# Optimization experiments

Hardware: AMD Instinct MI355X
Metric: run time of the kernel (lower is better)

The kernel has to match this reference:

```python
import jax, jax.numpy as jnp
import numpy as np

NUM_TOKENS = 16384
DIM = 4096
N_EXPERTS = 256
ROUTE_SCALE = 1.0


def setup_inputs() -> dict:
    key = jax.random.key(0)
    k_x, k_w = jax.random.split(key)
    x = jax.random.normal(k_x, (NUM_TOKENS, DIM), dtype=jnp.float32)
    # nn.init.normal_(weight, std=0.02)
    weight = 0.02 * jax.random.normal(k_w, (N_EXPERTS, DIM), dtype=jnp.float32)
    return {"x": x, "weight": weight}


def reference(x, weight):
    # Router GEMM: [T, D] @ [D, E] -> [T, E]
    scores = jnp.einsum("td,ed->te", x, weight)
    # Eval-mode token_choice path: softmax in fp32
    probs = jax.nn.softmax(scores.astype(jnp.float32), axis=-1)  # [T, E]
    indices = jnp.argmax(probs, axis=-1, keepdims=True)  # [T, 1] int
    # Hard one-hot scatter of argmax
    y_hard = jax.nn.one_hot(indices[:, 0], N_EXPERTS, dtype=probs.dtype)  # [T, E]
    # Straight-through estimator mix
    ste = jax.lax.stop_gradient(y_hard - probs) + probs
    # Gather routing weight at the selected expert
    weights = jnp.take_along_axis(ste, indices, axis=-1)  # [T, 1]
    weights = (weights * ROUTE_SCALE).astype(x.dtype)
    return weights, indices
```

## Files before the change

### kernel.cpp

```cpp
#include <hip/hip_runtime.h>
#include <stdint.h>

#define NUM_TOKENS 16384
#define DIM        4096
#define NEXP       256
#define MB         64
#define BK         64
#define APAD       72
#define NWAVES     8
#define MARGIN     0.025f
#define CAP        16384

typedef __attribute__((ext_vector_type(4))) float   f32x4;
typedef __attribute__((ext_vector_type(8))) __bf16  bf16x8;
typedef __attribute__((ext_vector_type(8))) unsigned short u16x8;

static __device__ __forceinline__ unsigned short f32_to_bf16(float f) {
    unsigned int u = __float_as_uint(f);
    u += 0x7fffu + ((u >> 16) & 1u);
    return (unsigned short)(u >> 16);
}

__global__ void cvt_weights(const float* __restrict__ w,
                            unsigned short* __restrict__ wh,
                            int* __restrict__ counter) {
    if (blockIdx.x == 0 && threadIdx.x == 0) *counter = 0;
    const int n4 = NEXP * DIM / 4;
    const int stride = gridDim.x * blockDim.x;
    for (int i = blockIdx.x * blockDim.x + threadIdx.x; i < n4; i += stride) {
        float4 v = ((const float4*)w)[i];
        ushort4 h;
        h.x = f32_to_bf16(v.x); h.y = f32_to_bf16(v.y);
        h.z = f32_to_bf16(v.z); h.w = f32_to_bf16(v.w);
        ((ushort4*)wh)[i] = h;
    }
}

__global__ __launch_bounds__(512, 2) void gate_main(
    const float* __restrict__ x,
    const unsigned short* __restrict__ wh,
    float* __restrict__ out,
    int* __restrict__ counter,
    int4* __restrict__ entries)
{
    __shared__ unsigned short lAh[2][MB][APAD];
    __shared__ unsigned short lBh[2][NEXP * BK];
    __shared__ float4 cand[NWAVES][MB];

    const int tid  = threadIdx.x;
    const int wv   = tid >> 6;
    const int lane = tid & 63;
    const int tok0 = blockIdx.x * MB;

    const int ta   = tid >> 3;
    const int kseg = (tid & 7) * 8;
    const float* xrow = x + (size_t)(tok0 + ta) * DIM + kseg;

    const int esub   = lane >> 3;
    const int bk_off = ((lane & 7) ^ esub) * 8;

    const int quad = lane >> 4;
    const int col  = lane & 15;

    f32x4 acc[4][2];
    #pragma unroll
    for (int mt = 0; mt < 4; ++mt) {
        acc[mt][0] = f32x4{0.f, 0.f, 0.f, 0.f};
        acc[mt][1] = f32x4{0.f, 0.f, 0.f, 0.f};
    }

    {
        #pragma unroll
        for (int jj = 0; jj < 4; ++jj) {
            const int e = jj * 64 + wv * 8 + esub;
            const unsigned short* gh = wh + (size_t)e * DIM + bk_off;
            unsigned short* dh = &lBh[0][jj * 4096 + wv * 512];
            __builtin_amdgcn_global_load_lds(
                (const __attribute__((address_space(1))) unsigned int*)gh,
                (__attribute__((address_space(3))) unsigned int*)dh, 16, 0, 0);
        }
        float4 v0 = *(const float4*)(xrow);
        float4 v1 = *(const float4*)(xrow + 4);
        u16x8 vh;
        vh[0] = f32_to_bf16(v0.x); vh[1] = f32_to_bf16(v0.y);
        vh[2] = f32_to_bf16(v0.z); vh[3] = f32_to_bf16(v0.w);
        vh[4] = f32_to_bf16(v1.x); vh[5] = f32_to_bf16(v1.y);
        vh[6] = f32_to_bf16(v1.z); vh[7] = f32_to_bf16(v1.w);
        *(u16x8*)&lAh[0][ta][kseg] = vh;
        __syncthreads();
    }

    int cur = 0;
    for (int k0 = 0; k0 < DIM; k0 += BK) {
        const int nxt = cur ^ 1;
        const bool has_next = (k0 + BK) < DIM;
        float4 v0, v1;

        if (has_next) {
            #pragma unroll
            for (int jj = 0; jj < 4; ++jj) {
                const int e = jj * 64 + wv * 8 + esub;
                const unsigned short* gh = wh + (size_t)e * DIM + (k0 + BK) + bk_off;
                unsigned short* dh = &lBh[nxt][jj * 4096 + wv * 512];
                __builtin_amdgcn_global_load_lds(
                    (const __attribute__((address_space(1))) unsigned int*)gh,
                    (__attribute__((address_space(3))) unsigned int*)dh, 16, 0, 0);
            }
            v0 = *(const float4*)(xrow + k0 + BK);
            v1 = *(const float4*)(xrow + k0 + BK + 4);
        }

        #pragma unroll
        for (int kk = 0; kk < BK; kk += 32) {
            const int kc = kk >> 3;
            bf16x8 ah[4], bh[2];
            #pragma unroll
            for (int mt = 0; mt < 4; ++mt)
                ah[mt] = *(const bf16x8*)&lAh[cur][mt * 16 + col][kk + quad * 8];
            #pragma unroll
            for (int nt = 0; nt < 2; ++nt) {
                const int e = wv * 32 + nt * 16 + col;
                const int cpos = (((kc + quad) ^ (e & 7)) * 8);
                bh[nt] = *(const bf16x8*)&lBh[cur][e * BK + cpos];
            }
            #pragma unroll
            for (int mt = 0; mt < 4; ++mt)
                #pragma unroll
                for (int nt = 0; nt < 2; ++nt)
                    acc[mt][nt] = __builtin_amdgcn_mfma_f32_16x16x32_bf16(
                        ah[mt], bh[nt], acc[mt][nt], 0, 0, 0);
        }

        if (has_next) {
            u16x8 vh;
            vh[0] = f32_to_bf16(v0.x); vh[1] = f32_to_bf16(v0.y);
            vh[2] = f32_to_bf16(v0.z); vh[3] = f32_to_bf16(v0.w);
            vh[4] = f32_to_bf16(v1.x); vh[5] = f32_to_bf16(v1.y);
            vh[6] = f32_to_bf16(v1.z); vh[7] = f32_to_bf16(v1.w);
            *(u16x8*)&lAh[nxt][ta][kseg] = vh;
        }
        __syncthreads();
        cur = nxt;
    }

    #pragma unroll
    for (int mt = 0; mt < 4; ++mt) {
        #pragma unroll
        for (int r = 0; r < 4; ++r) {
            float s0 = acc[mt][0][r]; int e0 = wv * 32 + col;
            float s1 = acc[mt][1][r]; int e1 = e0 + 16;
            float t1s, t2s; int t1e, t2e;
            if (s1 > s0) { t1s = s1; t1e = e1; t2s = s0; t2e = e0; }
            else         { t1s = s0; t1e = e0; t2s = s1; t2e = e1; }
            #pragma unroll
            for (int m = 1; m <= 8; m <<= 1) {
                float o1s = __shfl_xor(t1s, m); int o1e = __shfl_xor(t1e, m);
                float o2s = __shfl_xor(t2s, m); int o2e = __shfl_xor(t2e, m);
                bool o1_top = (o1s > t1s) || (o1s == t1s && o1e < t1e);
                if (o1_top) {
                    bool keep_t1 = (t1s > o2s) || (t1s == o2s && t1e < o2e);
                    t2s = keep_t1 ? t1s : o2s; t2e = keep_t1 ? t1e : o2e;
                    t1s = o1s; t1e = o1e;
                } else {
                    bool o1_2nd = (o1s > t2s) || (o1s == t2s && o1e < t2e);
                    if (o1_2nd) { t2s = o1s; t2e = o1e; }
                }
            }
            if (col == 0) {
                int tok = mt * 16 + quad * 4 + r;
                cand[wv][tok] = make_float4(t1s, __int_as_float(t1e), t2s, __int_as_float(t2e));
            }
        }
    }
    __syncthreads();

    if (tid < MB) {
        float4 c0 = cand[0][tid];
        float t1s = c0.x; int t1e = __float_as_int(c0.y);
        float t2s = c0.z; int t2e = __float_as_int(c0.w);
        #pragma unroll
        for (int wvi = 1; wvi < NWAVES; ++wvi) {
            float4 c = cand[wvi][tid];
            float o1s = c.x; int o1e = __float_as_int(c.y);
            float o2s = c.z; int o2e = __float_as_int(c.w);
            bool o1_top = (o1s > t1s) || (o1s == t1s && o1e < t1e);
            if (o1_top) {
                bool keep_t1 = (t1s > o2s) || (t1s == o2s && t1e < o2e);
                t2s = keep_t1 ? t1s : o2s; t2e = keep_t1 ? t1e : o2e;
                t1s = o1s; t1e = o1e;
            } else {
                bool o1_2nd = (o1s > t2s) || (o1s == t2s && o1e < t2e);
                if (o1_2nd) { t2s = o1s; t2e = o1e; }
            }
        }
        const int gtok = tok0 + tid;
        out[gtok] = 1.0f;
        out[NUM_TOKENS + gtok] = (float)t1e;
        if (t1s - t2s < MARGIN) {
            int slot = atomicAdd(counter, 1);
            if (slot < CAP) entries[slot] = make_int4(gtok, t1e, t2e, 0);
        }
    }
}

__global__ void refine(const float* __restrict__ x,
                       const float* __restrict__ w,
                       const int* __restrict__ counter,
                       const int4* __restrict__ entries,
                       float* __restrict__ out) {
    const int gwave  = (blockIdx.x * blockDim.x + threadIdx.x) >> 6;
    const int lane   = threadIdx.x & 63;
    const int nwaves = (gridDim.x * blockDim.x) >> 6;
    int n = *counter; if (n > CAP) n = CAP;
    for (int i = gwave; i < n; i += nwaves) {
        int4 e = entries[i];
        const float* xr = x + (size_t)e.x * DIM;
        const float* w1 = w + (size_t)e.y * DIM;
        const float* w2 = w + (size_t)e.z * DIM;
        double d1 = 0.0, d2 = 0.0;
        for (int k = lane; k < DIM; k += 64) {
            double xv = (double)xr[k];
            d1 += xv * (double)w1[k];
            d2 += xv * (double)w2[k];
        }
        #pragma unroll
        for (int m = 32; m > 0; m >>= 1) {
            d1 += __shfl_xor(d1, m);
            d2 += __shfl_xor(d2, m);
        }
        if (lane == 0) {
            int best = (d1 > d2) ? e.y : ((d2 > d1) ? e.z : (e.y < e.z ? e.y : e.z));
            out[NUM_TOKENS + e.x] = (float)best;
        }
    }
}

extern "C" void kernel_launch(void* const* d_in, const int* in_sizes, int n_in,
                              void* d_out, int out_size, void* d_ws, size_t ws_size,
                              hipStream_t stream) {
    const float* x = (const float*)d_in[0];
    const float* w = (const float*)d_in[1];
    float* out = (float*)d_out;

    char* ws = (char*)d_ws;
    unsigned short* wh = (unsigned short*)ws;
    int*  counter = (int*)(ws + (size_t)NEXP * DIM * 2);
    int4* entries = (int4*)(ws + (size_t)NEXP * DIM * 2 + 16);

    cvt_weights<<<256, 256, 0, stream>>>(w, wh, counter);
    gate_main<<<NUM_TOKENS / MB, 512, 0, stream>>>(x, wh, out, counter, entries);
    refine<<<256, 256, 0, stream>>>(x, w, counter, entries, out);
}
```

Measured before the change: 440.4 us.

## Split-K router GEMM across two blocks with separate top-2 reduction kernel

Splits the K dimension in half so each 64-token tile is processed by two blocks that write fp32 partial scores to workspace. A new reduce_top2 kernel sums the halves and does the top-2 selection and margin flagging. The main kernel also moves from 512 to 256 threads with single-buffered LDS and 64 experts per wave, which roughly halves LDS per block so more blocks can fit per CU. The cost is 32 MB of partial-score writes and reads, plus an extra launch, and the double-buffered prefetch overlap is lost.

```diff
diff --git a/kernel.cpp b/kernel.cpp
--- a/kernel.cpp
+++ b/kernel.cpp
@@ -6,8 +6,9 @@
 #define NEXP       256
 #define MB         64
 #define BK         64
+#define KHALF      2048
+#define NITER      (KHALF / BK)
 #define APAD       72
-#define NWAVES     8
 #define MARGIN     0.025f
 #define CAP        16384
 
@@ -36,25 +37,25 @@
     }
 }
 
-__global__ __launch_bounds__(512, 2) void gate_main(
+__global__ __launch_bounds__(256, 3) void gate_main(
     const float* __restrict__ x,
     const unsigned short* __restrict__ wh,
-    float* __restrict__ out,
-    int* __restrict__ counter,
-    int4* __restrict__ entries)
+    float* __restrict__ ps)
 {
-    __shared__ unsigned short lAh[2][MB][APAD];
-    __shared__ unsigned short lBh[2][NEXP * BK];
-    __shared__ float4 cand[NWAVES][MB];
+    __shared__ unsigned short lAh[MB][APAD];
+    __shared__ unsigned short lBh[NEXP * BK];
 
     const int tid  = threadIdx.x;
     const int wv   = tid >> 6;
     const int lane = tid & 63;
-    const int tok0 = blockIdx.x * MB;
-
-    const int ta   = tid >> 3;
-    const int kseg = (tid & 7) * 8;
-    const float* xrow = x + (size_t)(tok0 + ta) * DIM + kseg;
+    const int tile = blockIdx.x >> 1;
+    const int half = blockIdx.x & 1;
+    const int tok0 = tile * MB;
+    const int kbase = half * KHALF;
+
+    const int ta   = tid >> 2;
+    const int kseg = (tid & 3) * 16;
+    const float* xrow = x + (size_t)(tok0 + ta) * DIM + kbase + kseg;
 
     const int esub   = lane >> 3;
     const int bk_off = ((lane & 7) ^ esub) * 8;
@@ -62,127 +63,111 @@
     const int quad = lane >> 4;
     const int col  = lane & 15;
 
-    f32x4 acc[4][2];
+    f32x4 acc[4][4];
     #pragma unroll
-    for (int mt = 0; mt < 4; ++mt) {
-        acc[mt][0] = f32x4{0.f, 0.f, 0.f, 0.f};
-        acc[mt][1] = f32x4{0.f, 0.f, 0.f, 0.f};
-    }
-
-    {
-        #pragma unroll
-        for (int jj = 0; jj < 4; ++jj) {
-            const int e = jj * 64 + wv * 8 + esub;
-            const unsigned short* gh = wh + (size_t)e * DIM + bk_off;
-            unsigned short* dh = &lBh[0][jj * 4096 + wv * 512];
+    for (int mt = 0; mt < 4; ++mt)
+        #pragma unroll
+        for (int nt = 0; nt < 4; ++nt)
+            acc[mt][nt] = f32x4{0.f, 0.f, 0.f, 0.f};
+
+    float4 xv0 = *(const float4*)(xrow);
+    float4 xv1 = *(const float4*)(xrow + 4);
+    float4 xv2 = *(const float4*)(xrow + 8);
+    float4 xv3 = *(const float4*)(xrow + 12);
+
+    for (int it = 0; it < NITER; ++it) {
+        const int k0 = it * BK;
+
+        #pragma unroll
+        for (int jj = 0; jj < 8; ++jj) {
+            const int e = wv * 64 + jj * 8 + esub;
+            const unsigned short* gh = wh + (size_t)e * DIM + kbase + k0 + bk_off;
+            unsigned short* dh = &lBh[(wv * 64 + jj * 8) * BK];
             __builtin_amdgcn_global_load_lds(
                 (const __attribute__((address_space(1))) unsigned int*)gh,
                 (__attribute__((address_space(3))) unsigned int*)dh, 16, 0, 0);
         }
-        float4 v0 = *(const float4*)(xrow);
-        float4 v1 = *(const float4*)(xrow + 4);
-        u16x8 vh;
-        vh[0] = f32_to_bf16(v0.x); vh[1] = f32_to_bf16(v0.y);
-        vh[2] = f32_to_bf16(v0.z); vh[3] = f32_to_bf16(v0.w);
-        vh[4] = f32_to_bf16(v1.x); vh[5] = f32_to_bf16(v1.y);
-        vh[6] = f32_to_bf16(v1.z); vh[7] = f32_to_bf16(v1.w);
-        *(u16x8*)&lAh[0][ta][kseg] = vh;
+
+        {
+            u16x8 h0, h1;
+            h0[0] = f32_to_bf16(xv0.x); h0[1] = f32_to_bf16(xv0.y);
+            h0[2] = f32_to_bf16(xv0.z); h0[3] = f32_to_bf16(xv0.w);
+            h0[4] = f32_to_bf16(xv1.x); h0[5] = f32_to_bf16(xv1.y);
+            h0[6] = f32_to_bf16(xv1.z); h0[7] = f32_to_bf16(xv1.w);
+            h1[0] = f32_to_bf16(xv2.x); h1[1] = f32_to_bf16(xv2.y);
+            h1[2] = f32_to_bf16(xv2.z); h1[3] = f32_to_bf16(xv2.w);
+            h1[4] = f32_to_bf16(xv3.x); h1[5] = f32_to_bf16(xv3.y);
+            h1[6] = f32_to_bf16(xv3.z); h1[7] = f32_to_bf16(xv3.w);
+            *(u16x8*)&lAh[ta][kseg]     = h0;
+            *(u16x8*)&lAh[ta][kseg + 8] = h1;
+        }
         __syncthreads();
-    }
-
-    int cur = 0;
-    for (int k0 = 0; k0 < DIM; k0 += BK) {
-        const int nxt = cur ^ 1;
-        const bool has_next = (k0 + BK) < DIM;
-        float4 v0, v1;
-
-        if (has_next) {
-            #pragma unroll
-            for (int jj = 0; jj < 4; ++jj) {
-                const int e = jj * 64 + wv * 8 + esub;
-                const unsigned short* gh = wh + (size_t)e * DIM + (k0 + BK) + bk_off;
-                unsigned short* dh = &lBh[nxt][jj * 4096 + wv * 512];
-                __builtin_amdgcn_global_load_lds(
-                    (const __attribute__((address_space(1))) unsigned int*)gh,
-                    (__attribute__((address_space(3))) unsigned int*)dh, 16, 0, 0);
-            }
-            v0 = *(const float4*)(xrow + k0 + BK);
-            v1 = *(const float4*)(xrow + k0 + BK + 4);
+
+        if (it + 1 < NITER) {
+            xv0 = *(const float4*)(xrow + (it + 1) * BK);
+            xv1 = *(const float4*)(xrow + (it + 1) * BK + 4);
+            xv2 = *(const float4*)(xrow + (it + 1) * BK + 8);
+            xv3 = *(const float4*)(xrow + (it + 1) * BK + 12);
         }
 
         #pragma unroll
         for (int kk = 0; kk < BK; kk += 32) {
             const int kc = kk >> 3;
-            bf16x8 ah[4], bh[2];
+            bf16x8 ah[4], bh[4];
             #pragma unroll
             for (int mt = 0; mt < 4; ++mt)
-                ah[mt] = *(const bf16x8*)&lAh[cur][mt * 16 + col][kk + quad * 8];
-            #pragma unroll
-            for (int nt = 0; nt < 2; ++nt) {
-                const int e = wv * 32 + nt * 16 + col;
-                const int cpos = (((kc + quad) ^ (e & 7)) * 8);
-                bh[nt] = *(const bf16x8*)&lBh[cur][e * BK + cpos];
+                ah[mt] = *(const bf16x8*)&lAh[mt * 16 + col][kk + quad * 8];
+            #pragma unroll
+            for (int nt = 0; nt < 4; ++nt) {
+                const int e = wv * 64 + nt * 16 + col;
+                const int cpos = (((kc + quad) ^ (col & 7)) * 8);
+                bh[nt] = *(const bf16x8*)&lBh[e * BK + cpos];
             }
             #pragma unroll
             for (int mt = 0; mt < 4; ++mt)
                 #pragma unroll
-                for (int nt = 0; nt < 2; ++nt)
+                for (int nt = 0; nt < 4; ++nt)
                     acc[mt][nt] = __builtin_amdgcn_mfma_f32_16x16x32_bf16(
                         ah[mt], bh[nt], acc[mt][nt], 0, 0, 0);
         }
-
-        if (has_next) {
-            u16x8 vh;
-            vh[0] = f32_to_bf16(v0.x); vh[1] = f32_to_bf16(v0.y);
-            vh[2] = f32_to_bf16(v0.z); vh[3] = f32_to_bf16(v0.w);
-            vh[4] = f32_to_bf16(v1.x); vh[5] = f32_to_bf16(v1.y);
-            vh[6] = f32_to_bf16(v1.z); vh[7] = f32_to_bf16(v1.w);
-            *(u16x8*)&lAh[nxt][ta][kseg] = vh;
-        }
         __syncthreads();
-        cur = nxt;
-    }
-
+    }
+
+    float* base = ps + ((size_t)half * NUM_TOKENS + tok0) * NEXP;
     #pragma unroll
-    for (int mt = 0; mt < 4; ++mt) {
+    for (int mt = 0; mt < 4; ++mt)
         #pragma unroll
         for (int r = 0; r < 4; ++r) {
-            float s0 = acc[mt][0][r]; int e0 = wv * 32 + col;
-            float s1 = acc[mt][1][r]; int e1 = e0 + 16;
-            float t1s, t2s; int t1e, t2e;
-            if (s1 > s0) { t1s = s1; t1e = e1; t2s = s0; t2e = e0; }
-            else         { t1s = s0; t1e = e0; t2s = s1; t2e = e1; }
-            #pragma unroll
-            for (int m = 1; m <= 8; m <<= 1) {
-                float o1s = __shfl_xor(t1s, m); int o1e = __shfl_xor(t1e, m);
-                float o2s = __shfl_xor(t2s, m); int o2e = __shfl_xor(t2e, m);
-                bool o1_top = (o1s > t1s) || (o1s == t1s && o1e < t1e);
-                if (o1_top) {
-                    bool keep_t1 = (t1s > o2s) || (t1s == o2s && t1e < o2e);
-                    t2s = keep_t1 ? t1s : o2s; t2e = keep_t1 ? t1e : o2e;
-                    t1s = o1s; t1e = o1e;
-                } else {
-                    bool o1_2nd = (o1s > t2s) || (o1s == t2s && o1e < t2e);
-                    if (o1_2nd) { t2s = o1s; t2e = o1e; }
-                }
-            }
-            if (col == 0) {
-                int tok = mt * 16 + quad * 4 + r;
-                cand[wv][tok] = make_float4(t1s, __int_as_float(t1e), t2s, __int_as_float(t2e));
-            }
-        }
-    }
-    __syncthreads();
-
-    if (tid < MB) {
-        float4 c0 = cand[0][tid];
-        float t1s = c0.x; int t1e = __float_as_int(c0.y);
-        float t2s = c0.z; int t2e = __float_as_int(c0.w);
-        #pragma unroll
-        for (int wvi = 1; wvi < NWAVES; ++wvi) {
-            float4 c = cand[wvi][tid];
-            float o1s = c.x; int o1e = __float_as_int(c.y);
-            float o2s = c.z; int o2e = __float_as_int(c.w);
+            const int tok = mt * 16 + quad * 4 + r;
+            #pragma unroll
+            for (int nt = 0; nt < 4; ++nt)
+                base[(size_t)tok * NEXP + wv * 64 + nt * 16 + col] = acc[mt][nt][r];
+        }
+}
+
+__global__ void reduce_top2(const float* __restrict__ ps,
+                            float* __restrict__ out,
+                            int* __restrict__ counter,
+                            int4* __restrict__ entries) {
+    const int gw   = (blockIdx.x * blockDim.x + threadIdx.x) >> 6;
+    const int lane = threadIdx.x & 63;
+    const int nw   = (gridDim.x * blockDim.x) >> 6;
+    for (int t = gw; t < NUM_TOKENS; t += nw) {
+        const float4 a = *(const float4*)(ps + (size_t)t * NEXP + lane * 4);
+        const float4 b = *(const float4*)(ps + ((size_t)NUM_TOKENS + t) * NEXP + lane * 4);
+        float s[4] = {a.x + b.x, a.y + b.y, a.z + b.z, a.w + b.w};
+        float t1s = s[0]; int t1e = lane * 4;
+        float t2s = s[1]; int t2e = lane * 4 + 1;
+        if (t2s > t1s) { float ts = t1s; int te = t1e; t1s = t2s; t1e = t2e; t2s = ts; t2e = te; }
+        #pragma unroll
+        for (int j = 2; j < 4; ++j) {
+            if (s[j] > t1s)      { t2s = t1s; t2e = t1e; t1s = s[j]; t1e = lane * 4 + j; }
+            else if (s[j] > t2s) { t2s = s[j]; t2e = lane * 4 + j; }
+        }
+        #pragma unroll
+        for (int m = 1; m <= 32; m <<= 1) {
+            float o1s = __shfl_xor(t1s, m); int o1e = __shfl_xor(t1e, m);
+            float o2s = __shfl_xor(t2s, m); int o2e = __shfl_xor(t2e, m);
             bool o1_top = (o1s > t1s) || (o1s == t1s && o1e < t1e);
             if (o1_top) {
                 bool keep_t1 = (t1s > o2s) || (t1s == o2s && t1e < o2e);
@@ -193,12 +178,13 @@
                 if (o1_2nd) { t2s = o1s; t2e = o1e; }
             }
         }
-        const int gtok = tok0 + tid;
-        out[gtok] = 1.0f;
-        out[NUM_TOKENS + gtok] = (float)t1e;
-        if (t1s - t2s < MARGIN) {
-            int slot = atomicAdd(counter, 1);
-            if (slot < CAP) entries[slot] = make_int4(gtok, t1e, t2e, 0);
+        if (lane == 0) {
+            out[t] = 1.0f;
+            out[NUM_TOKENS + t] = (float)t1e;
+            if (t1s - t2s < MARGIN) {
+                int slot = atomicAdd(counter, 1);
+                if (slot < CAP) entries[slot] = make_int4(t, t1e, t2e, 0);
+            }
         }
     }
 }
@@ -244,10 +230,12 @@
 
     char* ws = (char*)d_ws;
     unsigned short* wh = (unsigned short*)ws;
-    int*  counter = (int*)(ws + (size_t)NEXP * DIM * 2);
-    int4* entries = (int4*)(ws + (size_t)NEXP * DIM * 2 + 16);
+    int*  counter = (int*)(ws + (2u << 20));
+    int4* entries = (int4*)(ws + (2u << 20) + 16);
+    float* ps     = (float*)(ws + (4u << 20));
 
     cvt_weights<<<256, 256, 0, stream>>>(w, wh, counter);
-    gate_main<<<NUM_TOKENS / MB, 512, 0, stream>>>(x, wh, out, counter, entries);
+    gate_main<<<2 * NUM_TOKENS / MB, 256, 0, stream>>>(x, wh, ps);
+    reduce_top2<<<512, 256, 0, stream>>>(ps, out, counter, entries);
     refine<<<256, 256, 0, stream>>>(x, w, counter, entries, out);
 }
```

After: 435.4 us. Within noise of the previous version (-1.1%).
